# Performance work log

Hardware: AMD Instinct MI355X
Metric: run time of the kernel (lower is better)

## Reference

```python
import jax, jax.numpy as jnp
import numpy as np
from jax import lax

STRIDES = (8, 16, 32)
NUM_CLASSES = 80
TOPK = 1000
CONF_THRESH = 0.05
NMS_THRESH = 0.6


def setup_inputs() -> dict:
    key = jax.random.key(0)
    ks = jax.random.split(key, 10)
    hw = [(256, 256), (128, 128), (64, 64)]
    inp = {}
    for lv, (h, w) in enumerate(hw):
        inp[f"cls_pred_{lv}"] = jax.random.normal(ks[3 * lv + 0], (NUM_CLASSES, h, w), jnp.float32)
        inp[f"reg_pred_{lv}"] = jax.random.normal(ks[3 * lv + 1], (4, h, w), jnp.float32)
        inp[f"ctn_pred_{lv}"] = jax.random.normal(ks[3 * lv + 2], (1, h, w), jnp.float32)
    inp["scales"] = jax.random.uniform(ks[9], (3,), jnp.float32)
    return inp


def _level_decode(cls_p, reg_p, ctn_p, scale, stride):
    # cls_p: [C,H,W] -> flatten to [M,C] matching torch permute(1,2,0).view(-1,C)
    C, H, W = cls_p.shape
    cls = jnp.transpose(cls_p, (1, 2, 0)).reshape(-1, C)          # [M,C]
    reg = jnp.transpose(reg_p, (1, 2, 0)).reshape(-1, 4)          # [M,4]
    reg = jax.nn.relu(reg * scale) * stride                       # Scale + relu + stride
    ctn = jnp.transpose(ctn_p, (1, 2, 0)).reshape(-1, 1)          # [M,1]
    joint = jnp.sqrt(jax.nn.sigmooid(cls) * jax.nn.sigmoid(ctn)) if False else \
        jnp.sqrt(jax.nn.sigmoid(cls) * jax.nn.sigmoid(ctn))      # [M,C]
    scores = jnp.max(joint, axis=-1)                              # [M]
    labels = jnp.argmax(joint, axis=-1)                           # [M]
    ay, ax = jnp.meshgrid(jnp.arange(H), jnp.arange(W), indexing='ij')
    anchors = (jnp.stack([ax, ay], -1).reshape(-1, 2).astype(cls.dtype) + 0.5) * stride  # [M,2]
    # per-level topk (M > TOPK for all levels here)
    scores, idx = lax.top_k(scores, TOPK)
    labels = labels[idx]
    reg = reg[idx]
    anchors = anchors[idx]
    boxes = jnp.concatenate([anchors - reg[:, :2], anchors + reg[:, 2:]], axis=-1)  # x1y1x2y2
    return scores, labels, boxes


def _nms(boxes, scores):
    # Faithful port of the pure-python NMS: fixed-shape keep mask, sorted order.
    N = boxes.shape[0]
    order = jnp.argsort(-scores)
    b = boxes[order]
    x1, y1, x2, y2 = b[:, 0], b[:, 1], b[:, 2], b[:, 3]
    areas = (x2 - x1) * (y2 - y1)
    xx1 = jnp.maximum(x1[:, None], x1[None, :])
    yy1 = jnp.maximum(y1[:, None], y1[None, :])
    xx2 = jnp.minimum(x2[:, None], x2[None, :])
    yy2 = jnp.minimum(y2[:, None], y2[None, :])
    w = jnp.maximum(1e-10, xx2 - xx1)
    h = jnp.maximum(1e-10, yy2 - yy1)
    inter = w * h
    iou = inter / (areas[:, None] + areas[None, :] - inter + 1e-14)  # [N,N]
    idxs = jnp.arange(N)

    def body(i, keep):
        sup = (iou[i] > NMS_THRESH) & (idxs > i) & keep[i]
        return keep & ~sup

    keep = lax.fori_loop(0, N, body, jnp.ones((N,), bool))
    return order, keep


def reference(cls_pred_0, cls_pred_1, cls_pred_2,
              reg_pred_0, reg_pred_1, reg_pred_2,
              ctn_pred_0, ctn_pred_1, ctn_pred_2, scales):
    cls_l = [cls_pred_0, cls_pred_1, cls_pred_2]
    reg_l = [reg_pred_0, reg_pred_1, reg_pred_2]
    ctn_l = [ctn_pred_0, ctn_pred_1, ctn_pred_2]
    all_s, all_l, all_b = [], [], []
    for lv in range(3):
        s, lb, bx = _level_decode(cls_l[lv], reg_l[lv], ctn_l[lv], scales[lv], float(STRIDES[lv]))
        all_s.append(s); all_l.append(lb); all_b.append(bx)
    scores = jnp.concatenate(all_s)   # [3000]
    labels = jnp.concatenate(all_l)
    boxes = jnp.concatenate(all_b)    # [3000,4]
    order, keep = _nms(boxes, scores)
    scores_s = scores[order]
    labels_s = labels[order]
    boxes_s = boxes[order]
    keep = keep & (scores_s > CONF_THRESH)
    return boxes_s, scores_s, labels_s, keep
```

## Files before the change

kernel.cpp:

```cpp
#include <hip/hip_runtime.h>
#include <cmath>
#include <stdint.h>

#define NPTS   86016
#define NCB    1024
#define K_TOP  1000
#define NOUT   3000
#define NWORDS 47
#define NTILE  47
#define CAND_CAP 16384
#define ECAP   8192
#define FCAP   1024
#define SPPB   64

#define CH_OFF     0
#define CNT_OFF    (NCB * 3 * 4)
#define MEMSET_BYTES (CNT_OFF + 64)
#define KEYS_OFF   (CNT_OFF + 64)
#define LAB_OFF    (KEYS_OFF + NPTS * 8)
#define SURE_OFF   (LAB_OFF + NPTS * 4)
#define CAND_OFF   (SURE_OFF + 3 * 1024 * 8)
#define SURV_OFF   (CAND_OFF + 3 * CAND_CAP * 8)
#define EDGE_OFF   (SURV_OFF + NOUT * 8 + 64)
#define FLAG_OFF   (EDGE_OFF + ECAP * 4)
#define SMERGE_OFF (FLAG_OFF + FCAP * 4)

__device__ __forceinline__ float sig_f32_stepwise(float x) {
    float e = (float)exp(-(double)x);
    return 1.0f / (1.0f + e);
}

__device__ __forceinline__ void locate(int g, int& lv, int& p, int& HW) {
    if (g < 65536)      { lv = 0; p = g;         HW = 65536; }
    else if (g < 81920) { lv = 1; p = g - 65536; HW = 16384; }
    else                { lv = 2; p = g - 81920; HW = 4096;  }
}

__global__ __launch_bounds__(256) void score_kernel(
        const float* __restrict__ cls0, const float* __restrict__ cls1,
        const float* __restrict__ cls2,
        const float* __restrict__ ctn0, const float* __restrict__ ctn1,
        const float* __restrict__ ctn2,
        unsigned long long* __restrict__ keys, int* __restrict__ labels,
        int* __restrict__ chist,
        int* __restrict__ cnt, unsigned* __restrict__ flags) {
    __shared__ float pm[5 * SPPB], pv[5 * SPPB];
    __shared__ int pidx[5 * SPPB];
    __shared__ int lch[NCB];
    const int tid = threadIdx.x;
    const int base = blockIdx.x * SPPB;
    for (int i = tid; i < NCB; i += 256) lch[i] = 0;
    for (int it = tid; it < 5 * SPPB; it += 256) {
        int c = it / SPPB, pt = it - c * SPPB;
        int g = base + pt, lv, p, HW;
        locate(g, lv, p, HW);
        const float* cls = (lv == 0) ? cls0 : ((lv == 1) ? cls1 : cls2);
        const float* bp = cls + (size_t)c * 16 * HW + p;
        float x[16];
#pragma unroll
        for (int cc = 0; cc < 16; cc++) x[cc] = bp[(size_t)cc * HW];
        float m = -INFINITY, v = -INFINITY; int idx = 0;
#pragma unroll
        for (int cc = 0; cc < 16; cc++)
            if (x[cc] > m) { v = m; m = x[cc]; idx = c * 16 + cc; }
        pm[it] = m; pv[it] = v; pidx[it] = idx;
    }
    __syncthreads();
    if (tid < SPPB) {
        int g = base + tid, lv, p, HW;
        locate(g, lv, p, HW);
        const float* ctn = (lv == 0) ? ctn0 : ((lv == 1) ? ctn1 : ctn2);
        float m = -INFINITY, v = -INFINITY; int idx = 0;
#pragma unroll
        for (int k = 0; k < 5; k++) {
            float bm = pm[k * SPPB + tid];
            float bv = pv[k * SPPB + tid];
            int bidx = pidx[k * SPPB + tid];
            if (bm > m) { v = fmaxf(m, bv); m = bm; idx = bidx; }
        }
        float sc = sig_f32_stepwise(ctn[p]);
        float sM = sig_f32_stepwise(m);
        float jm = __fsqrt_rn(sM * sc);
        float sV = sig_f32_stepwise(v);
        float jv = __fsqrt_rn(sV * sc);
        if (jv == jm) {
            int f = atomicAdd(&cnt[13], 1);
            if (f < FCAP) flags[f] = (unsigned)g;
        }
        unsigned int bits = __float_as_uint(jm);
        keys[g] = ((unsigned long long)bits << 32) | (0xFFFFFFFFu - (unsigned)g);
        labels[g] = idx;
        atomicAdd(&lch[(int)(bits >> 20)], 1);
    }
    __syncthreads();
    int lv0, p0, HW0; locate(base, lv0, p0, HW0);
    for (int i = tid; i < NCB; i += 256) {
        int v = lch[i];
        if (v) atomicAdd(&chist[lv0 * NCB + i], v);
    }
}

__global__ __launch_bounds__(1024) void tcs_kernel(
        const float* __restrict__ cls0, const float* __restrict__ cls1,
        const float* __restrict__ cls2,
        const float* __restrict__ ctn0, const float* __restrict__ ctn1,
        const float* __restrict__ ctn2,
        const unsigned long long* __restrict__ keys,
        const int* __restrict__ chist,
        const unsigned* __restrict__ flags, const int* __restrict__ cnt,
        int* __restrict__ labels,
        unsigned long long* __restrict__ sure,
        unsigned long long* __restrict__ cand,
        unsigned long long* __restrict__ surv) {
    int bid = blockIdx.x, tid = threadIdx.x;
    if (bid == 3) {
        int nf = cnt[13]; if (nf > FCAP) nf = FCAP;
        int wave = tid >> 6, lane = tid & 63;
        for (int f = wave; f < nf; f += 16) {
            int g = (int)flags[f], lv, p, HW;
            locate(g, lv, p, HW);
            const float* cls = (lv == 0) ? cls0 : ((lv == 1) ? cls1 : cls2);
            const float* ctn = (lv == 0) ? ctn0 : ((lv == 1) ? ctn1 : ctn2);
            float sc = sig_f32_stepwise(ctn[p]);
            float bestv = -1.0f; int besti = 127;
            {
                float s = sig_f32_stepwise(cls[(size_t)lane * HW + p]);
                float sj = __fsqrt_rn(s * sc);
                bestv = sj; besti = lane;
            }
            if (lane < 16) {
                int c2 = lane + 64;
                float s = sig_f32_stepwise(cls[(size_t)c2 * HW + p]);
                float sj = __fsqrt_rn(s * sc);
                if (sj > bestv) { bestv = sj; besti = c2; }
            }
            for (int off = 32; off; off >>= 1) {
                float ov = __shfl_xor(bestv, off, 64);
                int   oi = __shfl_xor(besti, off, 64);
                if (ov > bestv || (ov == bestv && oi < besti)) { bestv = ov; besti = oi; }
            }
            if (lane == 0) labels[g] = besti;
        }
        return;
    }
    const int lv = bid;
    const int base = (lv == 0) ? 0 : ((lv == 1) ? 65536 : 81920);
    const int HW = (lv == 0) ? 65536 : ((lv == 1) ? 16384 : 4096);
    __shared__ int part[1024];
    __shared__ int fine[257];
    __shared__ int s_chunk, s_above, sB, sR, sCnt2[2];
    __shared__ unsigned long long sel[1024];

    if (tid == 0) { sCnt2[0] = 0; sCnt2[1] = 0; }
    part[tid] = chist[lv * NCB + tid];
    __syncthreads();
    for (int off = 1; off < 1024; off <<= 1) {
        int v = part[tid] + ((tid + off < 1024) ? part[tid + off] : 0);
        __syncthreads(); part[tid] = v; __syncthreads();
    }
    int nxt = (tid < 1023) ? part[tid + 1] : 0;
    if (part[tid] >= K_TOP && nxt < K_TOP) { s_chunk = tid; s_above = nxt; }
    if (tid < 257) fine[tid] = 0;
    __syncthreads();
    const int chunk = s_chunk, above = s_above;
    for (int i = tid; i < HW; i += 1024) {
        unsigned bits = (unsigned)(keys[base + i] >> 32);
        if ((int)(bits >> 20) == chunk) atomicAdd(&fine[(bits >> 12) & 255], 1);
    }
    __syncthreads();
    for (int off = 1; off < 256; off <<= 1) {
        int v = 0;
        if (tid < 256) v = fine[tid] + ((tid + off < 256) ? fine[tid + off] : 0);
        __syncthreads(); if (tid < 256) fine[tid] = v; __syncthreads();
    }
    if (tid < 256) {
        int ge    = above + fine[tid];
        int genxt = above + ((tid < 255) ? fine[tid + 1] : 0);
        if (ge >= K_TOP && genxt < K_TOP) {
            sB = chunk * 256 + tid;
            sR = K_TOP - genxt;
        }
    }
    __syncthreads();
    const int B = sB;
    for (int i = tid; i < HW; i += 1024) {
        unsigned long long key = keys[base + i];
        int bin = (int)(key >> 44);
        if (bin > B) {
            int k = atomicAdd(&sCnt2[0], 1);
            sure[lv * 1024 + k] = key;
        } else if (bin == B) {
            int k = atomicAdd(&sCnt2[1], 1);
            if (k < CAND_CAP) cand[lv * CAND_CAP + k] = key;
        }
    }
    __syncthreads();
    unsigned long long* c = cand + lv * CAND_CAP;
    int n = sCnt2[1]; if (n > CAND_CAP) n = CAND_CAP;
    int R = sR;
    int Ca = K_TOP - R;
    int m = 1; while (m < n) m <<= 1;
    for (int t = n + tid; t < m; t += 1024) c[t] = 0ULL;
    __syncthreads();
    for (int k = 2; k <= m; k <<= 1)
        for (int j = k >> 1; j > 0; j >>= 1) {
            for (int t = tid; t < m; t += 1024) {
                int l = t ^ j;
                if (l > t) {
                    unsigned long long a = c[t], b = c[l];
                    if (((t & k) == 0) ? (a < b) : (a > b)) { c[t] = b; c[l] = a; }
                }
            }
            __syncthreads();
        }
    sel[tid] = (tid < Ca) ? sure[lv * 1024 + tid]
                          : ((tid < K_TOP) ? c[tid - Ca] : 0ULL);
    __syncthreads();
    for (int k = 2; k <= 1024; k <<= 1)
        for (int j = k >> 1; j > 0; j >>= 1) {
            int l = tid ^ j;
            if (l > tid) {
                unsigned long long a = sel[tid], b = sel[l];
                if (((tid & k) == 0) ? (a < b) : (a > b)) { sel[tid] = b; sel[l] = a; }
            }
            __syncthreads();
        }
    if (tid < K_TOP) surv[lv * K_TOP + tid] = sel[tid];
}

__global__ __launch_bounds__(1024) void merge_emit_kernel(
        const unsigned long long* __restrict__ surv,
        const int* __restrict__ labels,
        const float* __restrict__ reg0, const float* __restrict__ reg1,
        const float* __restrict__ reg2,
        const float* __restrict__ scales,
        float* __restrict__ out) {
    __shared__ unsigned long long L[3][1024];
    __shared__ unsigned long long s[NOUT];
    int tid = threadIdx.x;
#pragma unroll
    for (int lv = 0; lv < 3; lv++)
        L[lv][tid] = (tid < K_TOP) ? surv[lv * K_TOP + tid] : 0ULL;
    __syncthreads();
    for (int e = tid; e < NOUT; e += 1024) {
        int a = e / K_TOP, i = e - a * K_TOP;
        unsigned long long key = L[a][i];
        int rank = i;
#pragma unroll
        for (int b = 0; b < 3; b++) {
            if (b == a) continue;
            int lo = 0, hi = K_TOP;
            while (lo < hi) {
                int mid = (lo + hi) >> 1;
                if (L[b][mid] > key) lo = mid + 1; else hi = mid;
            }
            rank += lo;
        }
        s[rank] = key;
    }
    __syncthreads();
    for (int r = tid; r < NOUT; r += 1024) {
        unsigned long long key = s[r];
        unsigned int bits = (unsigned)(key >> 32);
        float score = __uint_as_float(bits);
        unsigned int g = 0xFFFFFFFFu - (unsigned)(key & 0xFFFFFFFFULL);
        int lv, p;
        if (g < 65536u)      { lv = 0; p = (int)g; }
        else if (g < 81920u) { lv = 1; p = (int)g - 65536; }
        else                 { lv = 2; p = (int)g - 81920; }
        const float* rp = (lv == 0) ? reg0 : ((lv == 1) ? reg1 : reg2);
        int HW = (lv == 0) ? 65536 : ((lv == 1) ? 16384 : 4096);
        int W = 256 >> lv;
        float strideF = (float)(8 << lv);
        float scale = scales[lv];
        int x = p & (W - 1);
        int y = p >> (8 - lv);
        float r0 = fmaxf(0.0f, rp[0 * HW + p] * scale) * strideF;
        float r1 = fmaxf(0.0f, rp[1 * HW + p] * scale) * strideF;
        float r2 = fmaxf(0.0f, rp[2 * HW + p] * scale) * strideF;
        float r3 = fmaxf(0.0f, rp[3 * HW + p] * scale) * strideF;
        float ax = ((float)x + 0.5f) * strideF;
        float ay = ((float)y + 0.5f) * strideF;
        out[r * 4 + 0] = ax - r0;
        out[r * 4 + 1] = ay - r1;
        out[r * 4 + 2] = ax + r2;
        out[r * 4 + 3] = ay + r3;
        out[12000 + r] = score;
        out[15000 + r] = (float)labels[g];
    }
}

__global__ __launch_bounds__(256) void edge_kernel(const float* __restrict__ out,
                                                   unsigned* __restrict__ edges_g,
                                                   int* __restrict__ cnt) {
    __shared__ float x1[128], y1[128], x2[128], y2[128];
    int t = blockIdx.x, tid = threadIdx.x;
    int ta = 0, rem = t;
    while (rem >= NTILE - ta) { rem -= NTILE - ta; ta++; }
    int tb = ta + rem;
    if (tid < 64) {
        int gi = ta * 64 + tid;
        if (gi < NOUT) {
            float4 b = ((const float4*)out)[gi];
            x1[tid] = b.x; y1[tid] = b.y; x2[tid] = b.z; y2[tid] = b.w;
        }
    } else if (tid < 128) {
        int gj = tb * 64 + (tid - 64);
        if (gj < NOUT) {
            float4 b = ((const float4*)out)[gj];
            x1[tid] = b.x; y1[tid] = b.y; x2[tid] = b.z; y2[tid] = b.w;
        }
    }
    __syncthreads();
#pragma unroll
    for (int q = 0; q < 16; q++) {
        int idx = q * 256 + tid;
        int ii = idx >> 6, jj = idx & 63;
        int i = ta * 64 + ii, j = tb * 64 + jj;
        if (i < j && j < NOUT) {
            float ai = (x2[ii] - x1[ii]) * (y2[ii] - y1[ii]);
            float aj = (x2[64 + jj] - x1[64 + jj]) * (y2[64 + jj] - y1[64 + jj]);
            float xx1 = fmaxf(x1[ii], x1[64 + jj]), yy1 = fmaxf(y1[ii], y1[64 + jj]);
            float xx2 = fminf(x2[ii], x2[64 + jj]), yy2 = fminf(y2[ii], y2[64 + jj]);
            float ww = fmaxf(1e-10f, xx2 - xx1);
            float hh = fmaxf(1e-10f, yy2 - yy1);
            float inter = ww * hh;
            float iou = inter / (((ai + aj) - inter) + 1e-14f);
            if ((double)iou > 0.6) {
                int e = atomicAdd(&cnt[12], 1);
                if (e < ECAP) edges_g[e] = ((unsigned)i << 12) | (unsigned)j;
            }
        }
    }
}

__global__ __launch_bounds__(1024) void nms_sparse_kernel(
        const unsigned* __restrict__ edges_g,
        const int* __restrict__ cnt,
        const float* __restrict__ scores_s,
        float* __restrict__ keep_out) {
    __shared__ unsigned ed[ECAP];
    __shared__ unsigned long long supLds[NWORDS];
    int tid = threadIdx.x;
    int E = cnt[12]; if (E > ECAP) E = ECAP;
    int m = 1; while (m < E) m <<= 1;
    for (int t = tid; t < m; t += 1024) ed[t] = (t < E) ? edges_g[t] : 0xFFFFFFFFu;
    __syncthreads();
    for (int k = 2; k <= m; k <<= 1)
        for (int j = k >> 1; j > 0; j >>= 1) {
            for (int t = tid; t < m; t += 1024) {
                int l = t ^ j;
                if (l > t) {
                    unsigned a = ed[t], b = ed[l];
                    if (((t & k) == 0) ? (a > b) : (a < b)) { ed[t] = b; ed[l] = a; }
                }
            }
            __syncthreads();
        }
    if (tid < 64) {
        int lane = tid;
        unsigned long long supW = 0ULL;
        int ep = 0;
        for (int c = 0; c < NWORDS; c++) {
            unsigned long long cw = __shfl(supW, c, 64);
            int hi = (c + 1) * 64;
            while (ep < E) {
                unsigned k = ed[ep];
                int i = (int)(k >> 12);
                if (i >= hi) break;
                int j = (int)(k & 4095);
                if (!((cw >> (i & 63)) & 1ULL)) {
                    if ((j >> 6) == c) cw |= 1ULL << (j & 63);
                    else if (lane == (j >> 6)) supW |= 1ULL << (j & 63);
                }
                ep++;
            }
            if (lane == c) supW = cw;
        }
        if (lane < NWORDS) supLds[lane] = supW;
    }
    __syncthreads();
    for (int j = tid; j < NOUT; j += 1024) {
        bool s = (supLds[j >> 6] >> (j & 63)) & 1ULL;
        float scv = scores_s[j];
        keep_out[j] = (!s && ((double)scv > 0.05)) ? 1.0f : 0.0f;
    }
}

extern "C" void kernel_launch(void* const* d_in, const int* in_sizes, int n_in,
                              void* d_out, int out_size, void* d_ws, size_t ws_size,
                              hipStream_t stream) {
    const float* cls0 = (const float*)d_in[0];
    const float* reg0 = (const float*)d_in[1];
    const float* ctn0 = (const float*)d_in[2];
    const float* cls1 = (const float*)d_in[3];
    const float* reg1 = (const float*)d_in[4];
    const float* ctn1 = (const float*)d_in[5];
    const float* cls2 = (const float*)d_in[6];
    const float* reg2 = (const float*)d_in[7];
    const float* ctn2 = (const float*)d_in[8];
    const float* scales = (const float*)d_in[9];

    char* ws = (char*)d_ws;
    int* chist = (int*)(ws + CH_OFF);
    int* cnt  = (int*)(ws + CNT_OFF);
    unsigned long long* keys = (unsigned long long*)(ws + KEYS_OFF);
    int* labels = (int*)(ws + LAB_OFF);
    unsigned long long* sure = (unsigned long long*)(ws + SURE_OFF);
    unsigned long long* cand = (unsigned long long*)(ws + CAND_OFF);
    unsigned long long* surv = (unsigned long long*)(ws + SURV_OFF);
    unsigned* edges = (unsigned*)(ws + EDGE_OFF);
    unsigned* flags = (unsigned*)(ws + FLAG_OFF);
    float* out = (float*)d_out;

    hipMemsetAsync(ws, 0, MEMSET_BYTES, stream);

    score_kernel<<<NPTS / SPPB, 256, 0, stream>>>(cls0, cls1, cls2, ctn0, ctn1, ctn2,
                                                  keys, labels, chist, cnt, flags);
    tcs_kernel<<<4, 1024, 0, stream>>>(cls0, cls1, cls2, ctn0, ctn1, ctn2,
                                       keys, chist, flags, cnt, labels,
                                       sure, cand, surv);
    merge_emit_kernel<<<1, 1024, 0, stream>>>(surv, labels, reg0, reg1, reg2, scales, out);
    edge_kernel<<<NTILE * (NTILE + 1) / 2, 256, 0, stream>>>(out, edges, cnt);
    nms_sparse_kernel<<<1, 1024, 0, stream>>>(edges, cnt, out + 12000, out + 18000);
}
```

Measured before the change: 192.9 us.

## Fuse top-k selection passes into one key scan with LDS sort

The per-level top-k selection now reads the key array once instead of twice. Keys above the coarse bin go straight into shared memory, and keys in the boundary coarse bin are staged to global memory for a small refinement pass. The global-memory bitonic sort of candidates followed by a second LDS sort is replaced by a single bitonic sort over a shared buffer of up to 4096 entries. This removes one full scan of up to 65536 keys per level and the global-memory sort traffic, in exchange for a larger shared-memory footprint and possible truncation if the boundary bin holds many entries.

```diff
diff --git a/kernel.cpp b/kernel.cpp
--- a/kernel.cpp
+++ b/kernel.cpp
@@ -8,22 +8,20 @@
 #define NOUT   3000
 #define NWORDS 47
 #define NTILE  47
-#define CAND_CAP 16384
 #define ECAP   8192
 #define FCAP   1024
 #define SPPB   64
+#define SELCAP 4096
 
 #define CH_OFF     0
 #define CNT_OFF    (NCB * 3 * 4)
 #define MEMSET_BYTES (CNT_OFF + 64)
 #define KEYS_OFF   (CNT_OFF + 64)
 #define LAB_OFF    (KEYS_OFF + NPTS * 8)
-#define SURE_OFF   (LAB_OFF + NPTS * 4)
-#define CAND_OFF   (SURE_OFF + 3 * 1024 * 8)
-#define SURV_OFF   (CAND_OFF + 3 * CAND_CAP * 8)
+#define STAGE_OFF  (LAB_OFF + NPTS * 4)
+#define SURV_OFF   (STAGE_OFF + 3 * 65536 * 8)
 #define EDGE_OFF   (SURV_OFF + NOUT * 8 + 64)
 #define FLAG_OFF   (EDGE_OFF + ECAP * 4)
-#define SMERGE_OFF (FLAG_OFF + FCAP * 4)
 
 __device__ __forceinline__ float sig_f32_stepwise(float x) {
     float e = (float)exp(-(double)x);
@@ -109,8 +107,7 @@
         const int* __restrict__ chist,
         const unsigned* __restrict__ flags, const int* __restrict__ cnt,
         int* __restrict__ labels,
-        unsigned long long* __restrict__ sure,
-        unsigned long long* __restrict__ cand,
+        unsigned long long* __restrict__ stage,
         unsigned long long* __restrict__ surv) {
     int bid = blockIdx.x, tid = threadIdx.x;
     if (bid == 3) {
@@ -146,12 +143,15 @@
     const int lv = bid;
     const int base = (lv == 0) ? 0 : ((lv == 1) ? 65536 : 81920);
     const int HW = (lv == 0) ? 65536 : ((lv == 1) ? 16384 : 4096);
+    unsigned long long* stg = stage + (size_t)lv * 65536;
+
     __shared__ int part[1024];
     __shared__ int fine[257];
-    __shared__ int s_chunk, s_above, sB, sR, sCnt2[2];
-    __shared__ unsigned long long sel[1024];
-
-    if (tid == 0) { sCnt2[0] = 0; sCnt2[1] = 0; }
+    __shared__ int s_chunk, s_above, sBf, sR;
+    __shared__ int sSure, sStage, sCand;
+    __shared__ unsigned long long sel[SELCAP];
+
+    if (tid == 0) { sSure = 0; sStage = 0; sCand = 0; }
     part[tid] = chist[lv * NCB + tid];
     __syncthreads();
     for (int off = 1; off < 1024; off <<= 1) {
@@ -164,8 +164,16 @@
     __syncthreads();
     const int chunk = s_chunk, above = s_above;
     for (int i = tid; i < HW; i += 1024) {
-        unsigned bits = (unsigned)(keys[base + i] >> 32);
-        if ((int)(bits >> 20) == chunk) atomicAdd(&fine[(bits >> 12) & 255], 1);
+        unsigned long long key = keys[base + i];
+        int cb = (int)(key >> 52);
+        if (cb > chunk) {
+            int k = atomicAdd(&sSure, 1);
+            sel[k] = key;
+        } else if (cb == chunk) {
+            int k = atomicAdd(&sStage, 1);
+            stg[k] = key;
+            atomicAdd(&fine[(int)(key >> 44) & 255], 1);
+        }
     }
     __syncthreads();
     for (int off = 1; off < 256; off <<= 1) {
@@ -177,51 +185,41 @@
         int ge    = above + fine[tid];
         int genxt = above + ((tid < 255) ? fine[tid + 1] : 0);
         if (ge >= K_TOP && genxt < K_TOP) {
-            sB = chunk * 256 + tid;
-            sR = K_TOP - genxt;
-        }
-    }
-    __syncthreads();
-    const int B = sB;
-    for (int i = tid; i < HW; i += 1024) {
-        unsigned long long key = keys[base + i];
-        int bin = (int)(key >> 44);
-        if (bin > B) {
-            int k = atomicAdd(&sCnt2[0], 1);
-            sure[lv * 1024 + k] = key;
-        } else if (bin == B) {
-            int k = atomicAdd(&sCnt2[1], 1);
-            if (k < CAND_CAP) cand[lv * CAND_CAP + k] = key;
-        }
-    }
-    __syncthreads();
-    unsigned long long* c = cand + lv * CAND_CAP;
-    int n = sCnt2[1]; if (n > CAND_CAP) n = CAND_CAP;
-    int R = sR;
-    int Ca = K_TOP - R;
-    int m = 1; while (m < n) m <<= 1;
-    for (int t = n + tid; t < m; t += 1024) c[t] = 0ULL;
+            sBf = tid;
+            sR  = K_TOP - genxt;
+        }
+    }
+    __syncthreads();
+    const int Bf = sBf;
+    const int nstage = sStage;
+    {
+        int Ca = above + ((Bf < 255) ? fine[Bf + 1] : 0);
+        for (int i = tid; i < nstage; i += 1024) {
+            unsigned long long key = stg[i];
+            int fb = (int)(key >> 44) & 255;
+            if (fb > Bf) {
+                int k = atomicAdd(&sSure, 1);
+                sel[k] = key;
+            } else if (fb == Bf) {
+                int k = atomicAdd(&sCand, 1);
+                int idx = Ca + k;
+                if (idx < SELCAP) sel[idx] = key;
+            }
+        }
+    }
+    __syncthreads();
+    int tot = sSure + sCand; if (tot > SELCAP) tot = SELCAP;
+    int m = 1024; while (m < tot) m <<= 1;
+    for (int t = tot + tid; t < m; t += 1024) sel[t] = 0ULL;
     __syncthreads();
     for (int k = 2; k <= m; k <<= 1)
         for (int j = k >> 1; j > 0; j >>= 1) {
             for (int t = tid; t < m; t += 1024) {
                 int l = t ^ j;
                 if (l > t) {
-                    unsigned long long a = c[t], b = c[l];
-                    if (((t & k) == 0) ? (a < b) : (a > b)) { c[t] = b; c[l] = a; }
+                    unsigned long long a = sel[t], b = sel[l];
+                    if (((t & k) == 0) ? (a < b) : (a > b)) { sel[t] = b; sel[l] = a; }
                 }
-            }
-            __syncthreads();
-        }
-    sel[tid] = (tid < Ca) ? sure[lv * 1024 + tid]
-                          : ((tid < K_TOP) ? c[tid - Ca] : 0ULL);
-    __syncthreads();
-    for (int k = 2; k <= 1024; k <<= 1)
-        for (int j = k >> 1; j > 0; j >>= 1) {
-            int l = tid ^ j;
-            if (l > tid) {
-                unsigned long long a = sel[tid], b = sel[l];
-                if (((tid & k) == 0) ? (a < b) : (a > b)) { sel[tid] = b; sel[l] = a; }
             }
             __syncthreads();
         }
@@ -406,8 +404,7 @@
     int* cnt  = (int*)(ws + CNT_OFF);
     unsigned long long* keys = (unsigned long long*)(ws + KEYS_OFF);
     int* labels = (int*)(ws + LAB_OFF);
-    unsigned long long* sure = (unsigned long long*)(ws + SURE_OFF);
-    unsigned long long* cand = (unsigned long long*)(ws + CAND_OFF);
+    unsigned long long* stage = (unsigned long long*)(ws + STAGE_OFF);
     unsigned long long* surv = (unsigned long long*)(ws + SURV_OFF);
     unsigned* edges = (unsigned*)(ws + EDGE_OFF);
     unsigned* flags = (unsigned*)(ws + FLAG_OFF);
@@ -419,7 +416,7 @@
                                                   keys, labels, chist, cnt, flags);
     tcs_kernel<<<4, 1024, 0, stream>>>(cls0, cls1, cls2, ctn0, ctn1, ctn2,
                                        keys, chist, flags, cnt, labels,
-                                       sure, cand, surv);
+                                       stage, surv);
     merge_emit_kernel<<<1, 1024, 0, stream>>>(surv, labels, reg0, reg1, reg2, scales, out);
     edge_kernel<<<NTILE * (NTILE + 1) / 2, 256, 0, stream>>>(out, edges, cnt);
     nms_sparse_kernel<<<1, 1024, 0, stream>>>(edges, cnt, out + 12000, out + 18000);
```

New measurement: 186.6 us. -3.3%, faster.
